# Kernel optimization log

Measured on AMD Instinct MI355X. Metric: run time of the kernel, lower is better.

## Reference

```python
import jax, jax.numpy as jnp
import numpy as np
import math

HID_DIM = 1024
NUM_HEADS = 8
QK_DIM = HID_DIM // 8  # 128 total, 16 per head


def setup_inputs() -> dict:
    key = jax.random.key(0)
    ks = jax.random.split(key, 7)
    B, M, C = 4, 2048, HID_DIM
    gain = math.sqrt(2.0)  # calculate_gain('relu')

    def xavier(k, fan_in, fan_out):
        std = gain * math.sqrt(2.0 / (fan_in + fan_out))
        a = math.sqrt(3.0) * std
        return jax.random.uniform(k, (fan_out, fan_in), jnp.float32, -a, a)

    x = jax.random.normal(ks[0], (B, M, C), jnp.float32)
    Wq = xavier(ks[1], C, QK_DIM)   # [out, in] like torch Linear
    Wk = xavier(ks[2], C, QK_DIM)
    Wv = xavier(ks[3], C, C)
    bq = jnp.zeros((QK_DIM,), jnp.float32)
    bk = jnp.zeros((QK_DIM,), jnp.float32)
    bv = jnp.zeros((C,), jnp.float32)
    gamma = jnp.zeros((1,), jnp.float32)
    return {"x": x, "Wq": Wq, "bq": bq, "Wk": Wk, "bk": bk,
            "Wv": Wv, "bv": bv, "gamma": gamma}


def reference(x, Wq, bq, Wk, bk, Wv, bv, gamma):
    B, M, C = x.shape
    H = NUM_HEADS
    dqk = QK_DIM // H   # per-head qk dim = 16
    dv = C // H         # per-head v dim = 128
    q = (x @ Wq.T + bq).reshape(B, M, H, dqk)  # [B,M,H,dqk]
    k = (x @ Wk.T + bk).reshape(B, M, H, dqk)
    v = (x @ Wv.T + bv).reshape(B, M, H, dv)
    scores = jnp.einsum('bmhd,bnhd->bhmn', q, k) / math.sqrt(dqk)
    scores = jnp.where(scores >= 0, scores, 0.2 * scores)  # LeakyReLU(0.2)
    beta = jax.nn.softmax(scores, axis=-1)                 # [B,H,M,M]
    out = jnp.einsum('bhmn,bnhd->bmhd', beta, v).reshape(B, M, C)
    return gamma * out + x
```

## Files before the change

### kernel.cpp

```cpp
#include <hip/hip_runtime.h>
#include <hip/hip_bf16.h>

typedef __bf16 bf16_t;
typedef __bf16 bf16x8 __attribute__((ext_vector_type(8)));
typedef float f32x4 __attribute__((ext_vector_type(4)));
typedef float f32x16 __attribute__((ext_vector_type(16)));

#define MTOT 8192
#define CDIM 1024
#define HEADS 8
#define DV 128
#define QKD 128
#define SEQ 2048
#define QSCALE 0.3606737602222409f

struct alignas(8) B4 { bf16_t a, b, c, d; };

__device__ inline bf16x8 cvt8(float4 a, float4 b) {
    bf16x8 v = { (bf16_t)a.x, (bf16_t)a.y, (bf16_t)a.z, (bf16_t)a.w,
                 (bf16_t)b.x, (bf16_t)b.y, (bf16_t)b.z, (bf16_t)b.w };
    return v;
}

__device__ inline void gl_lds16(const bf16_t* g, bf16_t* l) {
    __builtin_amdgcn_global_load_lds(
        (const __attribute__((address_space(1))) void*)g,
        (__attribute__((address_space(3))) void*)l, 16, 0, 0);
}

__device__ inline unsigned cvtpk(float a, float b) {
    unsigned r;
    asm("v_cvt_pk_bf16_f32 %0, %1, %2" : "=v"(r) : "v"(a), "v"(b));
    return r;
}

__device__ inline void plswap(unsigned& a, unsigned& b) {
    asm("v_permlane32_swap_b32 %0, %1" : "+v"(a), "+v"(b));
}

__global__ __launch_bounds__(256) void cvt_x(
    const float* __restrict__ src, bf16_t* __restrict__ dst, int n8)
{
    int i = blockIdx.x * blockDim.x + threadIdx.x;
    if (i >= n8) return;
    const float4* s = reinterpret_cast<const float4*>(src) + (size_t)i * 2;
    reinterpret_cast<bf16x8*>(dst)[i] = cvt8(s[0], s[1]);
}

__global__ __launch_bounds__(256) void cvt_w(
    const float* __restrict__ Wq, const float* __restrict__ Wk,
    const float* __restrict__ Wv, bf16_t* __restrict__ Wb)
{
    int i = blockIdx.x * blockDim.x + threadIdx.x;
    const float* src;
    if (i < 16384)       src = Wq + (size_t)i * 8;
    else if (i < 32768)  src = Wk + (size_t)(i - 16384) * 8;
    else                 src = Wv + (size_t)(i - 32768) * 8;
    const float4* s = reinterpret_cast<const float4*>(src);
    reinterpret_cast<bf16x8*>(Wb)[i] = cvt8(s[0], s[1]);
}

__global__ __launch_bounds__(256) void qkv_gemm3(
    const bf16_t* __restrict__ Xb, const bf16_t* __restrict__ Wb,
    const float* __restrict__ bq, const float* __restrict__ bk,
    const float* __restrict__ bv,
    bf16_t* __restrict__ Qw, bf16_t* __restrict__ Kw, bf16_t* __restrict__ Vt)
{
    __shared__ bf16_t As[128][64];
    __shared__ bf16_t Bs[128][64];

    const int tid = threadIdx.x;
    const int w = tid >> 6, l = tid & 63;
    const int c = l & 15, q = l >> 4;
    const int rw = w & 1, cw = w >> 1;

    const int lin = blockIdx.x + 10 * blockIdx.y;
    const int xcd = lin & 7, jj = lin >> 3;
    const int bx = jj % 10;
    const int m0 = (xcd * 8 + jj / 10) * 128;

    const bf16_t* Arow = Xb + (size_t)(m0 + w * 8 + (l >> 3)) * CDIM + (l & 7) * 8;
    const bf16_t* Brow = Wb + (size_t)(bx * 128 + w * 8 + (l >> 3)) * CDIM + (l & 7) * 8;

    f32x4 acc[16] = {};

    for (int k0 = 0; k0 < CDIM; k0 += 64) {
        __syncthreads();
        #pragma unroll
        for (int i = 0; i < 4; ++i) {
            gl_lds16(Arow + k0 + (size_t)i * 32 * CDIM, &As[i * 32 + w * 8][0]);
            gl_lds16(Brow + k0 + (size_t)i * 32 * CDIM, &Bs[i * 32 + w * 8][0]);
        }
        __syncthreads();
        #pragma unroll
        for (int kk = 0; kk < 2; ++kk) {
            bf16x8 af[4], bfr[4];
            #pragma unroll
            for (int mt = 0; mt < 4; ++mt)
                af[mt] = *(const bf16x8*)&As[rw * 64 + mt * 16 + c][kk * 32 + q * 8];
            #pragma unroll
            for (int nt = 0; nt < 4; ++nt)
                bfr[nt] = *(const bf16x8*)&Bs[cw * 64 + nt * 16 + c][kk * 32 + q * 8];
            #pragma unroll
            for (int mt = 0; mt < 4; ++mt)
                #pragma unroll
                for (int nt = 0; nt < 4; ++nt)
                    acc[mt * 4 + nt] = __builtin_amdgcn_mfma_f32_16x16x32_bf16(
                        af[mt], bfr[nt], acc[mt * 4 + nt], 0, 0, 0);
        }
    }

    #pragma unroll
    for (int mt = 0; mt < 4; ++mt)
        #pragma unroll
        for (int nt = 0; nt < 4; ++nt) {
            const int cl = cw * 64 + nt * 16 + c;
            f32x4 a = acc[mt * 4 + nt];
            const int mg = m0 + rw * 64 + mt * 16 + q * 4;
            if (bx == 0) {
                const float bb = bq[cl];
                #pragma unroll
                for (int r = 0; r < 4; ++r)
                    Qw[(size_t)(mg + r) * QKD + cl] = (bf16_t)((a[r] + bb) * QSCALE);
            } else if (bx == 1) {
                const float bb = bk[cl];
                #pragma unroll
                for (int r = 0; r < 4; ++r)
                    Kw[(size_t)(mg + r) * QKD + cl] = (bf16_t)(a[r] + bb);
            } else {
                const int h = bx - 2;
                const float bb = bv[h * DV + cl];
                const int bidx = mg >> 11, ml = mg & 2047;
                B4 v{ (bf16_t)(a[0] + bb), (bf16_t)(a[1] + bb),
                      (bf16_t)(a[2] + bb), (bf16_t)(a[3] + bb) };
                *(B4*)(Vt + ((size_t)(bidx * HEADS + h) * DV + cl) * SEQ + ml) = v;
            }
        }
}

__global__ __launch_bounds__(256, 2) void qkv_gemm2(
    const float* __restrict__ X,
    const float* __restrict__ Wq, const float* __restrict__ bq,
    const float* __restrict__ Wk, const float* __restrict__ bk,
    const float* __restrict__ Wv, const float* __restrict__ bv,
    bf16_t* __restrict__ Qw, bf16_t* __restrict__ Kw, bf16_t* __restrict__ Vt)
{
    __shared__ alignas(16) bf16_t As[128][72];
    __shared__ alignas(16) bf16_t Bs[128][72];

    const int tid  = threadIdx.x;
    const int lane = tid & 63, wave = tid >> 6;
    const int c = lane & 15, q = lane >> 4;
    const int rw = wave & 1, cw = wave >> 1;
    const int m0 = blockIdx.y * 128;
    const int nt_idx = blockIdx.x;

    const float* W; const float* bias;
    if (nt_idx == 0)      { W = Wq; bias = bq; }
    else if (nt_idx == 1) { W = Wk; bias = bk; }
    else { W = Wv + (size_t)(nt_idx - 2) * DV * CDIM; bias = bv + (nt_idx - 2) * DV; }

    const int srow = tid >> 1, sseg = tid & 1;
    const int swr = (srow >> 3) & 3;
    const float* ax = X + (size_t)(m0 + srow) * CDIM + sseg * 32;
    const float* bxp = W + (size_t)srow * CDIM + sseg * 32;

    f32x4 acc[16] = {};

    for (int k0 = 0; k0 < CDIM; k0 += 64) {
        __syncthreads();
        #pragma unroll
        for (int i = 0; i < 4; ++i) {
            const int ph = (sseg * 4 + i) ^ swr;
            *(bf16x8*)&As[srow][ph * 8] = cvt8(*(const float4*)(ax + k0 + i * 8),
                                               *(const float4*)(ax + k0 + i * 8 + 4));
            *(bf16x8*)&Bs[srow][ph * 8] = cvt8(*(const float4*)(bxp + k0 + i * 8),
                                               *(const float4*)(bxp + k0 + i * 8 + 4));
        }
        __syncthreads();
        #pragma unroll
        for (int kk = 0; kk < 2; ++kk) {
            bf16x8 af[4], bfr[4];
            #pragma unroll
            for (int mt = 0; mt < 4; ++mt) {
                const int row = rw * 64 + mt * 16 + c;
                af[mt] = *(const bf16x8*)&As[row][((kk * 4 + q) ^ ((row >> 3) & 3)) * 8];
            }
            #pragma unroll
            for (int nt = 0; nt < 4; ++nt) {
                const int row = cw * 64 + nt * 16 + c;
                bfr[nt] = *(const bf16x8*)&Bs[row][((kk * 4 + q) ^ ((row >> 3) & 3)) * 8];
            }
            #pragma unroll
            for (int mt = 0; mt < 4; ++mt)
                #pragma unroll
                for (int nt = 0; nt < 4; ++nt)
                    acc[mt * 4 + nt] = __builtin_amdgcn_mfma_f32_16x16x32_bf16(
                        af[mt], bfr[nt], acc[mt * 4 + nt], 0, 0, 0);
        }
    }

    #pragma unroll
    for (int mt = 0; mt < 4; ++mt)
        #pragma unroll
        for (int nt = 0; nt < 4; ++nt) {
            const int col = cw * 64 + nt * 16 + c;
            const float bb = bias[col];
            f32x4 a = acc[mt * 4 + nt];
            const int mg = m0 + rw * 64 + mt * 16 + q * 4;
            if (nt_idx == 0) {
                #pragma unroll
                for (int r = 0; r < 4; ++r)
                    Qw[(size_t)(mg + r) * QKD + col] = (bf16_t)((a[r] + bb) * QSCALE);
            } else if (nt_idx == 1) {
                #pragma unroll
                for (int r = 0; r < 4; ++r)
                    Kw[(size_t)(mg + r) * QKD + col] = (bf16_t)(a[r] + bb);
            } else {
                const int h = nt_idx - 2;
                const int bidx = mg >> 11, ml = mg & 2047;
                B4 v{ (bf16_t)(a[0] + bb), (bf16_t)(a[1] + bb),
                      (bf16_t)(a[2] + bb), (bf16_t)(a[3] + bb) };
                *(B4*)(Vt + ((size_t)(bidx * HEADS + h) * DV + col) * SEQ + ml) = v;
            }
        }
}

__global__ __launch_bounds__(256, 2) void attn3(
    const bf16_t* __restrict__ Q, const bf16_t* __restrict__ K,
    const bf16_t* __restrict__ Vt, const float* __restrict__ X,
    const float* __restrict__ gptr, float* __restrict__ out)
{
    __shared__ alignas(16) bf16_t Vs[2][128][72];

    const int tid  = threadIdx.x;
    const int lane = tid & 63;
    const int c5 = lane & 31, q1 = lane >> 5;

    const int lin = blockIdx.x + (SEQ / 128) * blockIdx.y;
    const int xcd = lin & 7, jj = lin >> 3;
    const int bh = xcd * 4 + (jj >> 4);
    const int qt = jj & 15;
    const int b = bh >> 3, h = bh & 7;
    const int wave = tid >> 6;
    const int mbase = qt * 128 + wave * 32;

    const bf16x8 qf = *(const bf16x8*)(
        Q + (size_t)(b * SEQ + mbase + c5) * QKD + h * 16 + q1 * 8);

    float li = 0.f;
    f32x16 o[4] = {};

    const bf16_t* Vhead = Vt + (size_t)(b * HEADS + h) * DV * SEQ;
    const bf16_t* Kbase = K + (size_t)(b * SEQ) * QKD + h * 16;

    const int sdv = tid >> 1, sseg = tid & 1;
    const int swv = (sdv >> 3) & 7;

    bf16x8 vA[4], vB[4], kA[2], kB[2];

    {
        const bf16_t* s0 = Vhead + (size_t)sdv * SEQ + sseg * 32;
        #pragma unroll
        for (int i = 0; i < 4; ++i) vA[i] = *(const bf16x8*)(s0 + i * 8);
        const bf16_t* s1 = s0 + 64;
        #pragma unroll
        for (int i = 0; i < 4; ++i) vB[i] = *(const bf16x8*)(s1 + i * 8);
        #pragma unroll
        for (int blk = 0; blk < 2; ++blk) {
            kA[blk] = *(const bf16x8*)(Kbase + (size_t)(blk * 32 + c5) * QKD + q1 * 8);
            kB[blk] = *(const bf16x8*)(Kbase + (size_t)(64 + blk * 32 + c5) * QKD + q1 * 8);
        }
        #pragma unroll
        for (int i = 0; i < 4; ++i) {
            const int ph = (sseg * 4 + i) ^ swv;
            *(bf16x8*)&Vs[0][sdv][ph * 8] = vA[i];
        }
        const bf16_t* s2 = s0 + 128;
        #pragma unroll
        for (int i = 0; i < 4; ++i) vA[i] = *(const bf16x8*)(s2 + i * 8);
    }

    union U8 { bf16x8 v; unsigned u[4]; };

    #pragma unroll 1
    for (int t = 0; t < 32; t += 2) {
        #pragma unroll
        for (int half = 0; half < 2; ++half) {
            __syncthreads();
            #pragma unroll
            for (int i = 0; i < 4; ++i) {
                const int ph = (sseg * 4 + i) ^ swv;
                *(bf16x8*)&Vs[half ? 0 : 1][sdv][ph * 8] = half ? vA[i] : vB[i];
            }
            const int cur = t + half;
            const bf16x8 k0f = half ? kB[0] : kA[0];
            const bf16x8 k1f = half ? kB[1] : kA[1];
            {
                const int vt  = (cur + 3 < 32) ? cur + 3 : 31;
                const int kt2 = (cur + 2 < 32) ? cur + 2 : 31;
                const bf16_t* src = Vhead + (size_t)sdv * SEQ + vt * 64 + sseg * 32;
                #pragma unroll
                for (int i = 0; i < 4; ++i) {
                    bf16x8 vv = *(const bf16x8*)(src + i * 8);
                    if (half) vA[i] = vv; else vB[i] = vv;
                }
                #pragma unroll
                for (int blk = 0; blk < 2; ++blk) {
                    bf16x8 kk = *(const bf16x8*)(
                        Kbase + (size_t)(kt2 * 64 + blk * 32 + c5) * QKD + q1 * 8);
                    if (half) kB[blk] = kk; else kA[blk] = kk;
                }
            }

            U8 frag[4];
            #pragma unroll
            for (int blk = 0; blk < 2; ++blk) {
                f32x16 z = {};
                f32x16 s = __builtin_amdgcn_mfma_f32_32x32x16_bf16(
                    blk ? k1f : k0f, qf, z, 0, 0, 0);
                float e[16];
                #pragma unroll
                for (int r = 0; r < 16; ++r) {
                    const float sv = s[r];
                    const float ev = __builtin_amdgcn_exp2f(fmaxf(sv, 0.2f * sv));
                    e[r] = ev;
                    li += ev;
                }
                unsigned w0 = cvtpk(e[0], e[1]),   w1 = cvtpk(e[2], e[3]);
                unsigned w2 = cvtpk(e[4], e[5]),   w3 = cvtpk(e[6], e[7]);
                unsigned w4 = cvtpk(e[8], e[9]),   w5 = cvtpk(e[10], e[11]);
                unsigned w6 = cvtpk(e[12], e[13]), w7 = cvtpk(e[14], e[15]);
                plswap(w0, w2); plswap(w1, w3);
                plswap(w4, w6); plswap(w5, w7);
                frag[blk * 2 + 0].u[0] = w0; frag[blk * 2 + 0].u[1] = w1;
                frag[blk * 2 + 0].u[2] = w2; frag[blk * 2 + 0].u[3] = w3;
                frag[blk * 2 + 1].u[0] = w4; frag[blk * 2 + 1].u[1] = w5;
                frag[blk * 2 + 1].u[2] = w6; frag[blk * 2 + 1].u[3] = w7;
            }

            __builtin_amdgcn_s_setprio(1);
            #pragma unroll
            for (int kt = 0; kt < 4; ++kt) {
                const bf16x8 pa = frag[kt].v;
                #pragma unroll
                for (int dvt = 0; dvt < 4; ++dvt) {
                    const int dv = dvt * 32 + c5;
                    const int phB = (kt * 2 + q1) ^ ((dv >> 3) & 7);
                    const bf16x8 vb = *(const bf16x8*)&Vs[half][dv][phB * 8];
                    o[dvt] = __builtin_amdgcn_mfma_f32_32x32x16_bf16(
                        pa, vb, o[dvt], 0, 0, 0);
                }
            }
            __builtin_amdgcn_s_setprio(0);
        }
    }

    li += __shfl_xor(li, 32);
    const float inv = 1.f / li;
    const float g = gptr[0];

    #pragma unroll
    for (int dvt = 0; dvt < 4; ++dvt)
        #pragma unroll
        for (int r = 0; r < 16; ++r) {
            const int row = (r & 3) + 8 * (r >> 2) + 4 * q1;
            const float linv = __shfl(inv, row);
            const size_t idx = (size_t)(b * SEQ + mbase + row) * CDIM
                             + h * DV + dvt * 32 + c5;
            out[idx] = g * (o[dvt][r] * linv) + X[idx];
        }
}

extern "C" void kernel_launch(void* const* d_in, const int* in_sizes, int n_in,
                              void* d_out, int out_size, void* d_ws, size_t ws_size,
                              hipStream_t stream) {
    const float* X  = (const float*)d_in[0];
    const float* Wq = (const float*)d_in[1];
    const float* bq = (const float*)d_in[2];
    const float* Wk = (const float*)d_in[3];
    const float* bk = (const float*)d_in[4];
    const float* Wv = (const float*)d_in[5];
    const float* bv = (const float*)d_in[6];
    const float* g  = (const float*)d_in[7];
    float* out = (float*)d_out;

    dim3 blk(256);
    const size_t big_elems = (size_t)MTOT * CDIM + 1280 * CDIM
                           + (size_t)MTOT * QKD * 2 + (size_t)MTOT * CDIM;
    const size_t big_ws = big_elems * sizeof(bf16_t);

    if (ws_size >= big_ws) {
        bf16_t* Xb = (bf16_t*)d_ws;
        bf16_t* Wb = Xb + (size_t)MTOT * CDIM;
        bf16_t* Qw = Wb + (size_t)1280 * CDIM;
        bf16_t* Kw = Qw + (size_t)MTOT * QKD;
        bf16_t* Vt = Kw + (size_t)MTOT * QKD;

        hipLaunchKernelGGL(cvt_x, dim3(MTOT * CDIM / 8 / 256), blk, 0, stream,
                           X, Xb, MTOT * CDIM / 8);
        hipLaunchKernelGGL(cvt_w, dim3(1280 * CDIM / 8 / 256), blk, 0, stream,
                           Wq, Wk, Wv, Wb);
        hipLaunchKernelGGL(qkv_gemm3, dim3(10, 64), blk, 0, stream,
                           Xb, Wb, bq, bk, bv, Qw, Kw, Vt);
        hipLaunchKernelGGL(attn3, dim3(SEQ / 128, 32), blk, 0, stream,
                           Qw, Kw, Vt, X, g, out);
    } else {
        bf16_t* Qw = (bf16_t*)d_ws;
        bf16_t* Kw = Qw + (size_t)MTOT * QKD;
        bf16_t* Vt = Kw + (size_t)MTOT * QKD;
        hipLaunchKernelGGL(qkv_gemm2, dim3(10, 64), blk, 0, stream,
                           X, Wq, bq, Wk, bk, Wv, bv, Qw, Kw, Vt);
        hipLaunchKernelGGL(attn3, dim3(SEQ / 128, 32), blk, 0, stream,
                           Qw, Kw, Vt, X, g, out);
    }
}
```

Measured before the change: 205.8 us.

## Double attention key tile to 128, merge convert kernels, drop GEMM XCD remap

The attention kernel now processes 128 keys per pipeline step instead of 64, which halves the number of barrier-separated iterations. It stages a larger V tile in LDS and interleaves the softmax fragment creation with the PV MFMAs per 32-key block. The two fp32-to-bf16 conversion kernels are merged into one launch to cut launch overhead. The QKV GEMM's XCD-aware block remapping is removed in favour of plain blockIdx mapping, which may hurt L2 locality. The larger LDS footprint and register usage may reduce occupancy.

```diff
diff --git a/kernel.cpp b/kernel.cpp
--- a/kernel.cpp
+++ b/kernel.cpp
@@ -38,26 +38,28 @@
     asm("v_permlane32_swap_b32 %0, %1" : "+v"(a), "+v"(b));
 }
 
-__global__ __launch_bounds__(256) void cvt_x(
-    const float* __restrict__ src, bf16_t* __restrict__ dst, int n8)
+#define XITEMS (MTOT * CDIM / 8)
+#define WITEMS (1280 * CDIM / 8)
+
+__global__ __launch_bounds__(256) void cvt_all(
+    const float* __restrict__ X,
+    const float* __restrict__ Wq, const float* __restrict__ Wk,
+    const float* __restrict__ Wv,
+    bf16_t* __restrict__ Xb, bf16_t* __restrict__ Wb)
 {
     int i = blockIdx.x * blockDim.x + threadIdx.x;
-    if (i >= n8) return;
-    const float4* s = reinterpret_cast<const float4*>(src) + (size_t)i * 2;
-    reinterpret_cast<bf16x8*>(dst)[i] = cvt8(s[0], s[1]);
-}
-
-__global__ __launch_bounds__(256) void cvt_w(
-    const float* __restrict__ Wq, const float* __restrict__ Wk,
-    const float* __restrict__ Wv, bf16_t* __restrict__ Wb)
-{
-    int i = blockIdx.x * blockDim.x + threadIdx.x;
-    const float* src;
-    if (i < 16384)       src = Wq + (size_t)i * 8;
-    else if (i < 32768)  src = Wk + (size_t)(i - 16384) * 8;
-    else                 src = Wv + (size_t)(i - 32768) * 8;
-    const float4* s = reinterpret_cast<const float4*>(src);
-    reinterpret_cast<bf16x8*>(Wb)[i] = cvt8(s[0], s[1]);
+    if (i < XITEMS) {
+        const float4* s = reinterpret_cast<const float4*>(X) + (size_t)i * 2;
+        reinterpret_cast<bf16x8*>(Xb)[i] = cvt8(s[0], s[1]);
+    } else {
+        int j = i - XITEMS;
+        const float* src;
+        if (j < 16384)       src = Wq + (size_t)j * 8;
+        else if (j < 32768)  src = Wk + (size_t)(j - 16384) * 8;
+        else                 src = Wv + (size_t)(j - 32768) * 8;
+        const float4* s = reinterpret_cast<const float4*>(src);
+        reinterpret_cast<bf16x8*>(Wb)[j] = cvt8(s[0], s[1]);
+    }
 }
 
 __global__ __launch_bounds__(256) void qkv_gemm3(
@@ -73,11 +75,8 @@
     const int w = tid >> 6, l = tid & 63;
     const int c = l & 15, q = l >> 4;
     const int rw = w & 1, cw = w >> 1;
-
-    const int lin = blockIdx.x + 10 * blockIdx.y;
-    const int xcd = lin & 7, jj = lin >> 3;
-    const int bx = jj % 10;
-    const int m0 = (xcd * 8 + jj / 10) * 128;
+    const int bx = blockIdx.x;
+    const int m0 = blockIdx.y * 128;
 
     const bf16_t* Arow = Xb + (size_t)(m0 + w * 8 + (l >> 3)) * CDIM + (l & 7) * 8;
     const bf16_t* Brow = Wb + (size_t)(bx * 128 + w * 8 + (l >> 3)) * CDIM + (l & 7) * 8;
@@ -231,7 +230,7 @@
     const bf16_t* __restrict__ Vt, const float* __restrict__ X,
     const float* __restrict__ gptr, float* __restrict__ out)
 {
-    __shared__ alignas(16) bf16_t Vs[2][128][72];
+    __shared__ alignas(16) bf16_t Vs[2][128][136];
 
     const int tid  = threadIdx.x;
     const int lane = tid & 63;
@@ -257,68 +256,66 @@
     const int sdv = tid >> 1, sseg = tid & 1;
     const int swv = (sdv >> 3) & 7;
 
-    bf16x8 vA[4], vB[4], kA[2], kB[2];
+    bf16x8 vreg[8];
+    bf16x8 kA[4], kB[4];
+
+    union U8 { bf16x8 v; unsigned u[4]; };
 
     {
-        const bf16_t* s0 = Vhead + (size_t)sdv * SEQ + sseg * 32;
-        #pragma unroll
-        for (int i = 0; i < 4; ++i) vA[i] = *(const bf16x8*)(s0 + i * 8);
-        const bf16_t* s1 = s0 + 64;
-        #pragma unroll
-        for (int i = 0; i < 4; ++i) vB[i] = *(const bf16x8*)(s1 + i * 8);
-        #pragma unroll
-        for (int blk = 0; blk < 2; ++blk) {
+        const bf16_t* s0 = Vhead + (size_t)sdv * SEQ + sseg * 64;
+        #pragma unroll
+        for (int i = 0; i < 8; ++i) vreg[i] = *(const bf16x8*)(s0 + i * 8);
+        #pragma unroll
+        for (int i = 0; i < 8; ++i) {
+            const int ph = (sseg * 8 + i) ^ swv;
+            *(bf16x8*)&Vs[0][sdv][ph * 8] = vreg[i];
+        }
+        const bf16_t* s1 = s0 + 128;
+        #pragma unroll
+        for (int i = 0; i < 8; ++i) vreg[i] = *(const bf16x8*)(s1 + i * 8);
+        #pragma unroll
+        for (int blk = 0; blk < 4; ++blk) {
             kA[blk] = *(const bf16x8*)(Kbase + (size_t)(blk * 32 + c5) * QKD + q1 * 8);
-            kB[blk] = *(const bf16x8*)(Kbase + (size_t)(64 + blk * 32 + c5) * QKD + q1 * 8);
-        }
-        #pragma unroll
-        for (int i = 0; i < 4; ++i) {
-            const int ph = (sseg * 4 + i) ^ swv;
-            *(bf16x8*)&Vs[0][sdv][ph * 8] = vA[i];
-        }
-        const bf16_t* s2 = s0 + 128;
-        #pragma unroll
-        for (int i = 0; i < 4; ++i) vA[i] = *(const bf16x8*)(s2 + i * 8);
-    }
-
-    union U8 { bf16x8 v; unsigned u[4]; };
+            kB[blk] = *(const bf16x8*)(Kbase + (size_t)(128 + blk * 32 + c5) * QKD + q1 * 8);
+        }
+    }
 
     #pragma unroll 1
-    for (int t = 0; t < 32; t += 2) {
+    for (int t = 0; t < 16; t += 2) {
         #pragma unroll
         for (int half = 0; half < 2; ++half) {
+            const int cur = t + half;
+            const int cbuf = cur & 1;
             __syncthreads();
-            #pragma unroll
-            for (int i = 0; i < 4; ++i) {
-                const int ph = (sseg * 4 + i) ^ swv;
-                *(bf16x8*)&Vs[half ? 0 : 1][sdv][ph * 8] = half ? vA[i] : vB[i];
-            }
-            const int cur = t + half;
-            const bf16x8 k0f = half ? kB[0] : kA[0];
-            const bf16x8 k1f = half ? kB[1] : kA[1];
+
+            #pragma unroll
+            for (int i = 0; i < 8; ++i) {
+                const int ph = (sseg * 8 + i) ^ swv;
+                *(bf16x8*)&Vs[cbuf ^ 1][sdv][ph * 8] = vreg[i];
+            }
             {
-                const int vt  = (cur + 3 < 32) ? cur + 3 : 31;
-                const int kt2 = (cur + 2 < 32) ? cur + 2 : 31;
-                const bf16_t* src = Vhead + (size_t)sdv * SEQ + vt * 64 + sseg * 32;
-                #pragma unroll
-                for (int i = 0; i < 4; ++i) {
-                    bf16x8 vv = *(const bf16x8*)(src + i * 8);
-                    if (half) vA[i] = vv; else vB[i] = vv;
-                }
-                #pragma unroll
-                for (int blk = 0; blk < 2; ++blk) {
+                const int vt = (cur + 2 < 16) ? cur + 2 : 15;
+                const bf16_t* src = Vhead + (size_t)sdv * SEQ + vt * 128 + sseg * 64;
+                #pragma unroll
+                for (int i = 0; i < 8; ++i) vreg[i] = *(const bf16x8*)(src + i * 8);
+            }
+            bf16x8 kf[4];
+            {
+                const int kt2 = (cur + 2 < 16) ? cur + 2 : 15;
+                #pragma unroll
+                for (int blk = 0; blk < 4; ++blk) {
+                    kf[blk] = half ? kB[blk] : kA[blk];
                     bf16x8 kk = *(const bf16x8*)(
-                        Kbase + (size_t)(kt2 * 64 + blk * 32 + c5) * QKD + q1 * 8);
+                        Kbase + (size_t)(kt2 * 128 + blk * 32 + c5) * QKD + q1 * 8);
                     if (half) kB[blk] = kk; else kA[blk] = kk;
                 }
             }
 
-            U8 frag[4];
-            #pragma unroll
-            for (int blk = 0; blk < 2; ++blk) {
+            #pragma unroll
+            for (int blk = 0; blk < 4; ++blk) {
                 f32x16 z = {};
                 f32x16 s = __builtin_amdgcn_mfma_f32_32x32x16_bf16(
-                    blk ? k1f : k0f, qf, z, 0, 0, 0);
+                    kf[blk], qf, z, 0, 0, 0);
                 float e[16];
                 #pragma unroll
                 for (int r = 0; r < 16; ++r) {
@@ -333,26 +330,26 @@
                 unsigned w6 = cvtpk(e[12], e[13]), w7 = cvtpk(e[14], e[15]);
                 plswap(w0, w2); plswap(w1, w3);
                 plswap(w4, w6); plswap(w5, w7);
-                frag[blk * 2 + 0].u[0] = w0; frag[blk * 2 + 0].u[1] = w1;
-                frag[blk * 2 + 0].u[2] = w2; frag[blk * 2 + 0].u[3] = w3;
-                frag[blk * 2 + 1].u[0] = w4; frag[blk * 2 + 1].u[1] = w5;
-                frag[blk * 2 + 1].u[2] = w6; frag[blk * 2 + 1].u[3] = w7;
-            }
-
-            __builtin_amdgcn_s_setprio(1);
-            #pragma unroll
-            for (int kt = 0; kt < 4; ++kt) {
-                const bf16x8 pa = frag[kt].v;
-                #pragma unroll
-                for (int dvt = 0; dvt < 4; ++dvt) {
-                    const int dv = dvt * 32 + c5;
-                    const int phB = (kt * 2 + q1) ^ ((dv >> 3) & 7);
-                    const bf16x8 vb = *(const bf16x8*)&Vs[half][dv][phB * 8];
-                    o[dvt] = __builtin_amdgcn_mfma_f32_32x32x16_bf16(
-                        pa, vb, o[dvt], 0, 0, 0);
+                U8 f0, f1;
+                f0.u[0] = w0; f0.u[1] = w1; f0.u[2] = w2; f0.u[3] = w3;
+                f1.u[0] = w4; f1.u[1] = w5; f1.u[2] = w6; f1.u[3] = w7;
+
+                __builtin_amdgcn_s_setprio(1);
+                #pragma unroll
+                for (int ktl = 0; ktl < 2; ++ktl) {
+                    const bf16x8 pa = ktl ? f1.v : f0.v;
+                    const int cchunk = (blk * 2 + ktl) * 2 + q1;
+                    #pragma unroll
+                    for (int dvt = 0; dvt < 4; ++dvt) {
+                        const int dv = dvt * 32 + c5;
+                        const int phB = cchunk ^ ((dv >> 3) & 7);
+                        const bf16x8 vb = *(const bf16x8*)&Vs[cbuf][dv][phB * 8];
+                        o[dvt] = __builtin_amdgcn_mfma_f32_32x32x16_bf16(
+                            pa, vb, o[dvt], 0, 0, 0);
+                    }
                 }
-            }
-            __builtin_amdgcn_s_setprio(0);
+                __builtin_amdgcn_s_setprio(0);
+            }
         }
     }
 
@@ -397,10 +394,8 @@
         bf16_t* Kw = Qw + (size_t)MTOT * QKD;
         bf16_t* Vt = Kw + (size_t)MTOT * QKD;
 
-        hipLaunchKernelGGL(cvt_x, dim3(MTOT * CDIM / 8 / 256), blk, 0, stream,
-                           X, Xb, MTOT * CDIM / 8);
-        hipLaunchKernelGGL(cvt_w, dim3(1280 * CDIM / 8 / 256), blk, 0, stream,
-                           Wq, Wk, Wv, Wb);
+        hipLaunchKernelGGL(cvt_all, dim3((XITEMS + WITEMS) / 256), blk, 0, stream,
+                           X, Wq, Wk, Wv, Xb, Wb);
         hipLaunchKernelGGL(qkv_gemm3, dim3(10, 64), blk, 0, stream,
                            Xb, Wb, bq, bk, bv, Qw, Kw, Vt);
         hipLaunchKernelGGL(attn3, dim3(SEQ / 128, 32), blk, 0, stream,
```

Measured after the change: 214.0 us. 1.04x slower.
